# Kernel optimization log

Measured on AMD Instinct MI355X. Metric: run time of the kernel, lower is better.

The kernel has to match this reference:

```python
import jax, jax.numpy as jnp
import numpy as np

N, E, D, H, L, G, C = 50000, 800000, 128, 128, 3, 128, 10
BN_EPS = 1e-5


def setup_inputs() -> dict:
    key = jax.random.key(0)
    ks = jax.random.split(key, 16)
    inp = {
        "x": jax.random.normal(ks[0], (N, D), dtype=jnp.float32),
        "node_centrality": jax.random.uniform(ks[1], (N,), dtype=jnp.float32),
        "edge_centrality": jax.random.uniform(ks[2], (E,), dtype=jnp.float32),
        # stacked per-layer MLP params (in == hidden so stackable)
        "W1": jax.random.normal(ks[3], (L, D, H), dtype=jnp.float32) * 0.05,
        "b1": jnp.zeros((L, H), dtype=jnp.float32),
        "g1": jnp.ones((L, H), dtype=jnp.float32),
        "be1": jnp.zeros((L, H), dtype=jnp.float32),
        "W2": jax.random.normal(ks[4], (L, H, H), dtype=jnp.float32) * 0.05,
        "b2": jnp.zeros((L, H), dtype=jnp.float32),
        "Wc": jax.random.normal(ks[5], (H, C), dtype=jnp.float32) * 0.05,
        "bc": jnp.zeros((C,), dtype=jnp.float32),
        "edge_index": jax.random.randint(ks[6], (2, E), 0, N, dtype=jnp.int64),
        "batch": jnp.sort(jax.random.randint(ks[7], (N,), 0, G, dtype=jnp.int64)),
    }
    return inp


def _gin_forward(x, node_centrality, edge_centrality, W1, b1, g1, be1, W2, b2, Wc, bc, edge_index, batch):
    src, dst = edge_index[0], edge_index[1]  # x_j = x[src], aggregate at dst
    ec = edge_centrality[:, None]
    nc = node_centrality[:, None]
    for l in range(L):
        # message: gather + scale by edge centrality; aggr='add': scatter-add
        msg = x[src] * ec                                      # [E, H]
        agg = jax.ops.segment_sum(msg, dst, num_segments=N)    # [N, H]
        h = agg * nc + x                                       # (1 + eps) * x_r, eps = 0
        # MLP([in, hidden, hidden]): Linear -> BatchNorm(train) -> ReLU -> Linear
        h = h @ W1[l] + b1[l]
        mu = h.mean(axis=0)
        var = h.var(axis=0)  # biased, matches BN training stats
        h = (h - mu) * jax.lax.rsqrt(var + BN_EPS) * g1[l] + be1[l]
        h = jax.nn.relu(h)
        h = h @ W2[l] + b2[l]
        x = jax.nn.relu(h)  # outer .relu() in GIN.forward
    # global mean pool over graphs
    sums = jax.ops.segment_sum(x, batch, num_segments=G)           # [G, H]
    cnt = jax.ops.segment_sum(jnp.ones((N,), x.dtype), batch, num_segments=G)
    pooled = sums / jnp.maximum(cnt, 1.0)[:, None]
    return pooled @ Wc + bc  # [G, C]


def reference(x, edge_index, batch, node_centrality, edge_centrality, W1, b1, g1, be1, W2, b2, Wc, bc):
    return _gin_forward(x, node_centrality, edge_centrality, W1, b1, g1, be1, W2, b2, Wc, bc, edge_index, batch)
```

## Files before the change

### kernel.cpp

```cpp
#include <hip/hip_runtime.h>
#include <hip/hip_fp16.h>

#define Nn 50000
#define Ee 800000
#define HD 128
#define Ll 3
#define Gg 128
#define Cc 10
#define BN_EPS 1e-5f
#define NBLK1 782
#define NPART 1564
#define PPAD 1600
#define NSCB 49

typedef __attribute__((ext_vector_type(8))) __bf16 bf16x8;
typedef __attribute__((ext_vector_type(4))) __bf16 bf16x4;
typedef __attribute__((ext_vector_type(2))) __bf16 bf16x2;
typedef __attribute__((ext_vector_type(4))) float f32x4;

__global__ void k_deg(const int* __restrict__ dst, int* __restrict__ deg) {
  int i = blockIdx.x * blockDim.x + threadIdx.x;
  int base = i * 4;
  if (base >= Ee) return;
#pragma unroll
  for (int j = 0; j < 4; ++j) {
    int e = base + j;
    if (e < Ee) atomicAdd(&deg[dst[e]], 1);
  }
}

__global__ void k_scan1(const int* __restrict__ deg, int* __restrict__ offs,
                        int* __restrict__ bsum) {
  __shared__ int b0[1024], b1[1024];
  int tid = threadIdx.x;
  int i = blockIdx.x * 1024 + tid;
  int v = (i < Nn) ? deg[i] : 0;
  int* cur = b0; int* nxt = b1;
  cur[tid] = v;
  __syncthreads();
  for (int off = 1; off < 1024; off <<= 1) {
    int s = cur[tid] + ((tid >= off) ? cur[tid - off] : 0);
    nxt[tid] = s;
    __syncthreads();
    int* t = cur; cur = nxt; nxt = t;
  }
  if (i < Nn) offs[i] = cur[tid] - v;
  if (tid == 1023) bsum[blockIdx.x] = cur[1023];
}

__global__ void k_scan2(const int* __restrict__ bsum, int* __restrict__ carry) {
  int lane = threadIdx.x;
  int v = (lane < NSCB) ? bsum[lane] : 0;
  int s = v;
  for (int off = 1; off < 64; off <<= 1) {
    int t = __shfl_up(s, off, 64);
    if (lane >= off) s += t;
  }
  if (lane < NSCB) carry[lane] = s - v;
}

__global__ void k_scan3(const int* __restrict__ carry, int* __restrict__ offs,
                        int* __restrict__ cursor) {
  int i = blockIdx.x * 1024 + threadIdx.x;
  if (i < Nn) {
    int o = offs[i] + carry[blockIdx.x];
    offs[i] = o; cursor[i] = o;
  }
  if (i == 0) offs[Nn] = Ee;
}

__global__ void k_fill(const int* __restrict__ src, const int* __restrict__ dst,
                       const float* __restrict__ ec, int* __restrict__ cursor,
                       unsigned int* __restrict__ epk) {
  int i = blockIdx.x * blockDim.x + threadIdx.x;
  int base = i * 4;
  if (base >= Ee) return;
  int d[4], s[4], p[4]; unsigned short hb[4]; bool ok[4];
#pragma unroll
  for (int j = 0; j < 4; ++j) {
    int e = base + j;
    ok[j] = e < Ee;
    if (ok[j]) {
      d[j] = dst[e]; s[j] = src[e];
      hb[j] = __half_as_ushort(__float2half(ec[e]));
    }
  }
#pragma unroll
  for (int j = 0; j < 4; ++j)
    if (ok[j]) p[j] = atomicAdd(&cursor[d[j]], 1);
#pragma unroll
  for (int j = 0; j < 4; ++j)
    if (ok[j]) __builtin_nontemporal_store(((unsigned int)s[j] << 16) | hb[j],
                                           &epk[p[j]]);
}

__global__ void k_xcast(const float* __restrict__ x, __bf16* __restrict__ xb) {
  int i = blockIdx.x * blockDim.x + threadIdx.x;
  int stride = gridDim.x * blockDim.x;
  const int n4 = Nn * 32;
  for (int t = i; t < n4; t += stride) {
    f32x4 v = ((const f32x4*)x)[t];
    bf16x4 b;
#pragma unroll
    for (int j = 0; j < 4; ++j) b[j] = (__bf16)v[j];
    ((bf16x4*)xb)[t] = b;
  }
}

__global__ void k_wprep(const float* __restrict__ W1, const float* __restrict__ W2,
                        __bf16* __restrict__ wtHi, __bf16* __restrict__ wtLo) {
  int mat = blockIdx.x >> 3;
  int chunk = blockIdx.x & 7;
  const float* W = (mat < 3) ? (W1 + mat * 16384) : (W2 + (mat - 3) * 16384);
  __bf16* hi = wtHi + mat * 16384;
  __bf16* lo = wtLo + mat * 16384;
  for (int t = threadIdx.x; t < 2048; t += blockDim.x) {
    int idx = chunk * 2048 + t;
    int n = idx >> 7, k = idx & 127;
    float v = W[k * 128 + n];
    __bf16 h = (__bf16)v;
    hi[idx] = h;
    lo[idx] = (__bf16)(v - (float)h);
  }
}

__global__ void k_agg(const __bf16* __restrict__ xb, const int* __restrict__ offs,
                      const unsigned int* __restrict__ epk, __bf16* __restrict__ aggb) {
  int wid = threadIdx.x >> 6, lane = threadIdx.x & 63;
  int n = blockIdx.x * 4 + wid;
  if (n >= Nn) return;
  int beg = offs[n], end = offs[n + 1];
  const unsigned int* x2 = (const unsigned int*)xb;
  float ax[8], ay[8];
#pragma unroll
  for (int t = 0; t < 8; ++t) { ax[t] = 0.f; ay[t] = 0.f; }
  int j = beg;
  for (; j + 7 < end; j += 8) {
    unsigned int e[8], v[8];
#pragma unroll
    for (int t = 0; t < 8; ++t) e[t] = epk[j + t];
#pragma unroll
    for (int t = 0; t < 8; ++t) v[t] = x2[(e[t] >> 16) * 64 + lane];
#pragma unroll
    for (int t = 0; t < 8; ++t) {
      __half_raw h; h.x = (unsigned short)(e[t] & 0xffffu);
      float w = __half2float(h);
      ax[t] = fmaf(__uint_as_float(v[t] << 16), w, ax[t]);
      ay[t] = fmaf(__uint_as_float(v[t] & 0xffff0000u), w, ay[t]);
    }
  }
  for (; j < end; ++j) {
    unsigned int e = epk[j];
    unsigned int v = x2[(e >> 16) * 64 + lane];
    __half_raw h; h.x = (unsigned short)(e & 0xffffu);
    float w = __half2float(h);
    ax[0] = fmaf(__uint_as_float(v << 16), w, ax[0]);
    ay[0] = fmaf(__uint_as_float(v & 0xffff0000u), w, ay[0]);
  }
  float sx = (ax[0] + ax[1]) + (ax[2] + ax[3]) + ((ax[4] + ax[5]) + (ax[6] + ax[7]));
  float sy = (ay[0] + ay[1]) + (ay[2] + ay[3]) + ((ay[4] + ay[5]) + (ay[6] + ay[7]));
  bf16x2 o; o[0] = (__bf16)sx; o[1] = (__bf16)sy;
  ((bf16x2*)aggb)[n * 64 + lane] = o;
}

__device__ __forceinline__ void split8(const float* a, bf16x8& hi, bf16x8& lo) {
#pragma unroll
  for (int j = 0; j < 8; ++j) {
    float v = a[j];
    __bf16 h = (__bf16)v;
    hi[j] = h;
    lo[j] = (__bf16)(v - (float)h);
  }
}

__launch_bounds__(256)
__global__ void k_gemm1(const __bf16* __restrict__ aggb, const float* __restrict__ nc,
                        const __bf16* __restrict__ xb,
                        const __bf16* __restrict__ wtHi, const __bf16* __restrict__ wtLo,
                        const float* __restrict__ bias, __bf16* __restrict__ h1b,
                        float* __restrict__ partial) {
  int tid = threadIdx.x;
  int w = tid >> 6, l = tid & 63;
  int wr = w >> 1, wc = w & 1;
  int row0 = blockIdx.x * 64 + wr * 32;
  int l15 = l & 15, lg = l >> 4;
  int colw = wc * 64;
  int krow = lg * 8;

  f32x4 acc[2][4];
#pragma unroll
  for (int m = 0; m < 2; ++m)
#pragma unroll
    for (int n = 0; n < 4; ++n) acc[m][n] = (f32x4){0.f, 0.f, 0.f, 0.f};

  int rowA[2]; bool rv[2]; float ncv[2];
#pragma unroll
  for (int m = 0; m < 2; ++m) {
    rowA[m] = row0 + m * 16 + l15;
    rv[m] = rowA[m] < Nn;
    ncv[m] = rv[m] ? nc[rowA[m]] : 0.f;
  }

#pragma unroll
  for (int ks = 0; ks < 4; ++ks) {
    int k0 = ks * 32 + krow;
    bf16x8 aHi[2], aLo[2];
#pragma unroll
    for (int m = 0; m < 2; ++m) {
      float av[8];
      if (rv[m]) {
        bf16x8 ag = *(const bf16x8*)(aggb + rowA[m] * 128 + k0);
        bf16x8 xv = *(const bf16x8*)(xb + rowA[m] * 128 + k0);
#pragma unroll
        for (int jj = 0; jj < 8; ++jj)
          av[jj] = fmaf((float)ag[jj], ncv[m], (float)xv[jj]);
      } else {
#pragma unroll
        for (int jj = 0; jj < 8; ++jj) av[jj] = 0.f;
      }
      split8(av, aHi[m], aLo[m]);
    }
    bf16x8 bHi[4], bLo[4];
#pragma unroll
    for (int n = 0; n < 4; ++n) {
      int c = colw + n * 16 + l15;
      bHi[n] = *(const bf16x8*)(wtHi + c * 128 + k0);
      bLo[n] = *(const bf16x8*)(wtLo + c * 128 + k0);
    }
#pragma unroll
    for (int m = 0; m < 2; ++m)
#pragma unroll
      for (int n = 0; n < 4; ++n) {
        acc[m][n] = __builtin_amdgcn_mfma_f32_16x16x32_bf16(aHi[m], bHi[n], acc[m][n], 0, 0, 0);
        acc[m][n] = __builtin_amdgcn_mfma_f32_16x16x32_bf16(aLo[m], bHi[n], acc[m][n], 0, 0, 0);
        acc[m][n] = __builtin_amdgcn_mfma_f32_16x16x32_bf16(aHi[m], bLo[n], acc[m][n], 0, 0, 0);
      }
  }

  float s[4] = {0.f, 0.f, 0.f, 0.f}, q[4] = {0.f, 0.f, 0.f, 0.f};
#pragma unroll
  for (int n = 0; n < 4; ++n) {
    int c = colw + n * 16 + l15;
    float bv = bias[c];
#pragma unroll
    for (int m = 0; m < 2; ++m) {
      int rbase = row0 + m * 16 + lg * 4;
#pragma unroll
      for (int r = 0; r < 4; ++r) {
        int rr = rbase + r;
        if (rr < Nn) {
          float o = acc[m][n][r] + bv;
          h1b[rr * 128 + c] = (__bf16)o;
          s[n] += o; q[n] += o * o;
        }
      }
    }
  }
#pragma unroll
  for (int n = 0; n < 4; ++n) {
    s[n] += __shfl_xor(s[n], 16, 64); q[n] += __shfl_xor(q[n], 16, 64);
    s[n] += __shfl_xor(s[n], 32, 64); q[n] += __shfl_xor(q[n], 32, 64);
  }
  if (lg == 0) {
    int slot = blockIdx.x * 2 + wr;
#pragma unroll
    for (int n = 0; n < 4; ++n) {
      int f = colw + n * 16 + l15;
      partial[f * PPAD + slot] = s[n];
      partial[(128 + f) * PPAD + slot] = q[n];
    }
  }
}

__global__ void k_bnfin(const float* __restrict__ partial,
                        const float* __restrict__ g1, const float* __restrict__ be1,
                        float* __restrict__ scaleA, float* __restrict__ shiftA) {
  __shared__ float ss[256], qq[256];
  int f = blockIdx.x, t = threadIdx.x;
  float s = 0.f, q = 0.f;
  for (int b = t; b < NPART; b += 256) {
    s += partial[f * PPAD + b];
    q += partial[(128 + f) * PPAD + b];
  }
  ss[t] = s; qq[t] = q;
  __syncthreads();
  for (int off = 128; off > 0; off >>= 1) {
    if (t < off) { ss[t] += ss[t + off]; qq[t] += qq[t + off]; }
    __syncthreads();
  }
  if (t == 0) {
    const float inv = 1.0f / (float)Nn;
    float mu = ss[0] * inv;
    float var = fmaxf(qq[0] * inv - mu * mu, 0.f);
    float rs = rsqrtf(var + BN_EPS);
    float sc = rs * g1[f];
    scaleA[f] = sc;
    shiftA[f] = be1[f] - mu * sc;
  }
}

__launch_bounds__(256)
__global__ void k_gemm2(const __bf16* __restrict__ h1b, const float* __restrict__ scaleA,
                        const float* __restrict__ shiftA,
                        const __bf16* __restrict__ wtHi, const __bf16* __restrict__ wtLo,
                        const float* __restrict__ bias, __bf16* __restrict__ xbout) {
  int tid = threadIdx.x;
  int w = tid >> 6, l = tid & 63;
  int wr = w >> 1, wc = w & 1;
  int row0 = blockIdx.x * 64 + wr * 32;
  int l15 = l & 15, lg = l >> 4;
  int colw = wc * 64;
  int krow = lg * 8;

  f32x4 acc[2][4];
#pragma unroll
  for (int m = 0; m < 2; ++m)
#pragma unroll
    for (int n = 0; n < 4; ++n) acc[m][n] = (f32x4){0.f, 0.f, 0.f, 0.f};

  int rowA[2]; bool rv[2];
#pragma unroll
  for (int m = 0; m < 2; ++m) {
    rowA[m] = row0 + m * 16 + l15;
    rv[m] = rowA[m] < Nn;
  }

#pragma unroll
  for (int ks = 0; ks < 4; ++ks) {
    int k0 = ks * 32 + krow;
    f32x4 sc0 = *(const f32x4*)(scaleA + k0), sc1 = *(const f32x4*)(scaleA + k0 + 4);
    f32x4 sh0 = *(const f32x4*)(shiftA + k0), sh1 = *(const f32x4*)(shiftA + k0 + 4);
    bf16x8 aHi[2], aLo[2];
#pragma unroll
    for (int m = 0; m < 2; ++m) {
      float av[8];
      if (rv[m]) {
        bf16x8 hv = *(const bf16x8*)(h1b + rowA[m] * 128 + k0);
#pragma unroll
        for (int jj = 0; jj < 4; ++jj) {
          av[jj]     = fmaxf(fmaf((float)hv[jj],     sc0[jj], sh0[jj]), 0.f);
          av[4 + jj] = fmaxf(fmaf((float)hv[4 + jj], sc1[jj], sh1[jj]), 0.f);
        }
      } else {
#pragma unroll
        for (int jj = 0; jj < 8; ++jj) av[jj] = 0.f;
      }
      split8(av, aHi[m], aLo[m]);
    }
    bf16x8 bHi[4], bLo[4];
#pragma unroll
    for (int n = 0; n < 4; ++n) {
      int c = colw + n * 16 + l15;
      bHi[n] = *(const bf16x8*)(wtHi + c * 128 + k0);
      bLo[n] = *(const bf16x8*)(wtLo + c * 128 + k0);
    }
#pragma unroll
    for (int m = 0; m < 2; ++m)
#pragma unroll
      for (int n = 0; n < 4; ++n) {
        acc[m][n] = __builtin_amdgcn_mfma_f32_16x16x32_bf16(aHi[m], bHi[n], acc[m][n], 0, 0, 0);
        acc[m][n] = __builtin_amdgcn_mfma_f32_16x16x32_bf16(aLo[m], bHi[n], acc[m][n], 0, 0, 0);
        acc[m][n] = __builtin_amdgcn_mfma_f32_16x16x32_bf16(aHi[m], bLo[n], acc[m][n], 0, 0, 0);
      }
  }

#pragma unroll
  for (int n = 0; n < 4; ++n) {
    int c = colw + n * 16 + l15;
    float bv = bias[c];
#pragma unroll
    for (int m = 0; m < 2; ++m) {
      int rbase = row0 + m * 16 + lg * 4;
#pragma unroll
      for (int r = 0; r < 4; ++r) {
        int rr = rbase + r;
        if (rr < Nn) xbout[rr * 128 + c] = (__bf16)fmaxf(acc[m][n][r] + bv, 0.f);
      }
    }
  }
}

#define PCH 64
__global__ void k_pool(const __bf16* __restrict__ xb, const int* __restrict__ batch,
                       float* __restrict__ pooled, float* __restrict__ gcnt) {
  int wid = threadIdx.x >> 6, lane = threadIdx.x & 63;
  int w = blockIdx.x * 4 + wid;
  int n0 = w * PCH;
  if (n0 >= Nn) return;
  int n1 = (n0 + PCH < Nn) ? n0 + PCH : Nn;
  const unsigned int* x2 = (const unsigned int*)xb;
  float2 acc = make_float2(0.f, 0.f);
  int cur = batch[n0];
  int cnt = 0;
  for (int n = n0; n < n1; ++n) {
    int g = batch[n];
    if (g != cur) {
      atomicAdd(&pooled[cur * 128 + lane * 2 + 0], acc.x);
      atomicAdd(&pooled[cur * 128 + lane * 2 + 1], acc.y);
      if (lane == 0) atomicAdd(&gcnt[cur], (float)cnt);
      acc = make_float2(0.f, 0.f); cnt = 0; cur = g;
    }
    unsigned int v = x2[n * 64 + lane];
    acc.x += __uint_as_float(v << 16);
    acc.y += __uint_as_float(v & 0xffff0000u);
    ++cnt;
  }
  atomicAdd(&pooled[cur * 128 + lane * 2 + 0], acc.x);
  atomicAdd(&pooled[cur * 128 + lane * 2 + 1], acc.y);
  if (lane == 0) atomicAdd(&gcnt[cur], (float)cnt);
}

__global__ void k_head(const float* __restrict__ pooled, const float* __restrict__ gcnt,
                       const float* __restrict__ Wc, const float* __restrict__ bc,
                       float* __restrict__ out) {
  __shared__ float p[128];
  int g = blockIdx.x, tid = threadIdx.x;
  p[tid] = pooled[g * 128 + tid] / fmaxf(gcnt[g], 1.0f);
  __syncthreads();
  if (tid < Cc) {
    float acc = bc[tid];
    for (int k = 0; k < 128; ++k) acc = fmaf(p[k], Wc[k * Cc + tid], acc);
    out[g * Cc + tid] = acc;
  }
}

extern "C" void kernel_launch(void* const* d_in, const int* in_sizes, int n_in,
                              void* d_out, int out_size, void* d_ws, size_t ws_size,
                              hipStream_t stream) {
  const float* x    = (const float*)d_in[0];
  const float* ncn  = (const float*)d_in[1];
  const float* ecn  = (const float*)d_in[2];
  const float* W1   = (const float*)d_in[3];
  const float* b1   = (const float*)d_in[4];
  const float* g1   = (const float*)d_in[5];
  const float* be1  = (const float*)d_in[6];
  const float* W2   = (const float*)d_in[7];
  const float* b2   = (const float*)d_in[8];
  const float* Wc   = (const float*)d_in[9];
  const float* bc   = (const float*)d_in[10];
  const int*   ei   = (const int*)d_in[11];
  const int*   batch= (const int*)d_in[12];
  const int* src  = ei;
  const int* dstp = ei + Ee;

  float* fws = (float*)d_ws;
  float* partial  = fws;
  float* scaleA   = partial + 256 * PPAD;
  float* shiftA   = scaleA + 128;
  float* pooled   = shiftA + 128;
  float* gcnt     = pooled + Gg * 128;
  int*   deg      = (int*)(gcnt + 128);
  int*   offs     = deg + Nn;
  int*   cursor   = offs + Nn + 64;
  int*   bsum     = cursor + Nn;
  int*   carry    = bsum + 64;
  unsigned int* epk = (unsigned int*)(carry + 64);
  __bf16* wtHi    = (__bf16*)(epk + Ee);
  __bf16* wtLo    = wtHi + 6 * 16384;
  __bf16* xb      = wtLo + 6 * 16384;
  __bf16* aggb    = xb + Nn * 128;
  __bf16* h1b     = aggb + Nn * 128;

  k_wprep<<<48, 256, 0, stream>>>(W1, W2, wtHi, wtLo);
  k_xcast<<<2048, 256, 0, stream>>>(x, xb);
  hipMemsetAsync(deg, 0, Nn * sizeof(int), stream);
  k_deg<<<(Ee / 4 + 255) / 256, 256, 0, stream>>>(dstp, deg);
  k_scan1<<<NSCB, 1024, 0, stream>>>(deg, offs, bsum);
  k_scan2<<<1, 64, 0, stream>>>(bsum, carry);
  k_scan3<<<NSCB, 1024, 0, stream>>>(carry, offs, cursor);
  k_fill<<<(Ee / 4 + 255) / 256, 256, 0, stream>>>(src, dstp, ecn, cursor, epk);

  for (int l = 0; l < Ll; ++l) {
    k_agg<<<(Nn + 3) / 4, 256, 0, stream>>>(xb, offs, epk, aggb);
    k_gemm1<<<NBLK1, 256, 0, stream>>>(aggb, ncn, xb,
                                       wtHi + l * 16384, wtLo + l * 16384,
                                       b1 + l * 128, h1b, partial);
    k_bnfin<<<128, 256, 0, stream>>>(partial, g1 + l * 128, be1 + l * 128,
                                     scaleA, shiftA);
    k_gemm2<<<NBLK1, 256, 0, stream>>>(h1b, scaleA, shiftA,
                                       wtHi + (3 + l) * 16384, wtLo + (3 + l) * 16384,
                                       b2 + l * 128, xb);
  }

  hipMemsetAsync(pooled, 0, (Gg * 128 + 128) * sizeof(float), stream);
  k_pool<<<(Nn + PCH * 4 - 1) / (PCH * 4), 256, 0, stream>>>(xb, batch, pooled, gcnt);
  k_head<<<Gg, 128, 0, stream>>>(pooled, gcnt, Wc, bc, (float*)d_out);
}
```

Before: 545.3 us.

## Fuse neighbor aggregation into first GEMM via LDS and drop A-lo MFMA passes

Removes the separate aggregation kernel: each GEMM1 block now gathers and sums neighbor rows for its 64 nodes, combines them with the self term, and stages the bf16 A tile in swizzled shared memory before the MFMA loop. This avoids writing and re-reading the aggregate buffer and saves one launch per layer. Both GEMMs also drop the low-part A split, using a bf16 A operand with hi/lo weights (2 MFMAs instead of 3), which lowers precision. The edge-fill store is made a regular store instead of nontemporal. Risk: the gather phase runs with only 782 blocks, so latency hiding may be worse than in the dedicated aggregation kernel.

Result: slower. 592.8 us (+8.7%).

```diff
diff --git a/kernel.cpp b/kernel.cpp
--- a/kernel.cpp
+++ b/kernel.cpp
@@ -90,8 +90,7 @@
     if (ok[j]) p[j] = atomicAdd(&cursor[d[j]], 1);
 #pragma unroll
   for (int j = 0; j < 4; ++j)
-    if (ok[j]) __builtin_nontemporal_store(((unsigned int)s[j] << 16) | hb[j],
-                                           &epk[p[j]]);
+    if (ok[j]) epk[p[j]] = ((unsigned int)s[j] << 16) | hb[j];
 }
 
 __global__ void k_xcast(const float* __restrict__ x, __bf16* __restrict__ xb) {
@@ -124,68 +123,66 @@
   }
 }
 
-__global__ void k_agg(const __bf16* __restrict__ xb, const int* __restrict__ offs,
-                      const unsigned int* __restrict__ epk, __bf16* __restrict__ aggb) {
-  int wid = threadIdx.x >> 6, lane = threadIdx.x & 63;
-  int n = blockIdx.x * 4 + wid;
-  if (n >= Nn) return;
-  int beg = offs[n], end = offs[n + 1];
-  const unsigned int* x2 = (const unsigned int*)xb;
-  float ax[8], ay[8];
-#pragma unroll
-  for (int t = 0; t < 8; ++t) { ax[t] = 0.f; ay[t] = 0.f; }
-  int j = beg;
-  for (; j + 7 < end; j += 8) {
-    unsigned int e[8], v[8];
-#pragma unroll
-    for (int t = 0; t < 8; ++t) e[t] = epk[j + t];
-#pragma unroll
-    for (int t = 0; t < 8; ++t) v[t] = x2[(e[t] >> 16) * 64 + lane];
-#pragma unroll
-    for (int t = 0; t < 8; ++t) {
-      __half_raw h; h.x = (unsigned short)(e[t] & 0xffffu);
-      float w = __half2float(h);
-      ax[t] = fmaf(__uint_as_float(v[t] << 16), w, ax[t]);
-      ay[t] = fmaf(__uint_as_float(v[t] & 0xffff0000u), w, ay[t]);
-    }
-  }
-  for (; j < end; ++j) {
-    unsigned int e = epk[j];
-    unsigned int v = x2[(e >> 16) * 64 + lane];
-    __half_raw h; h.x = (unsigned short)(e & 0xffffu);
-    float w = __half2float(h);
-    ax[0] = fmaf(__uint_as_float(v << 16), w, ax[0]);
-    ay[0] = fmaf(__uint_as_float(v & 0xffff0000u), w, ay[0]);
-  }
-  float sx = (ax[0] + ax[1]) + (ax[2] + ax[3]) + ((ax[4] + ax[5]) + (ax[6] + ax[7]));
-  float sy = (ay[0] + ay[1]) + (ay[2] + ay[3]) + ((ay[4] + ay[5]) + (ay[6] + ay[7]));
-  bf16x2 o; o[0] = (__bf16)sx; o[1] = (__bf16)sy;
-  ((bf16x2*)aggb)[n * 64 + lane] = o;
-}
-
-__device__ __forceinline__ void split8(const float* a, bf16x8& hi, bf16x8& lo) {
-#pragma unroll
-  for (int j = 0; j < 8; ++j) {
-    float v = a[j];
-    __bf16 h = (__bf16)v;
-    hi[j] = h;
-    lo[j] = (__bf16)(v - (float)h);
-  }
-}
-
 __launch_bounds__(256)
-__global__ void k_gemm1(const __bf16* __restrict__ aggb, const float* __restrict__ nc,
-                        const __bf16* __restrict__ xb,
+__global__ void k_gemm1(const __bf16* __restrict__ xb, const float* __restrict__ nc,
+                        const int* __restrict__ offs, const unsigned int* __restrict__ epk,
                         const __bf16* __restrict__ wtHi, const __bf16* __restrict__ wtLo,
                         const float* __restrict__ bias, __bf16* __restrict__ h1b,
                         float* __restrict__ partial) {
+  __shared__ unsigned int Als[64 * 64];
   int tid = threadIdx.x;
   int w = tid >> 6, l = tid & 63;
+  int row0 = blockIdx.x * 64;
+  const unsigned int* x2 = (const unsigned int*)xb;
+
+  for (int it = 0; it < 16; ++it) {
+    int n = row0 + w * 16 + it;
+    float sx = 0.f, sy = 0.f;
+    if (n < Nn) {
+      int beg = offs[n], end = offs[n + 1];
+      float ax[8], ay[8];
+#pragma unroll
+      for (int t = 0; t < 8; ++t) { ax[t] = 0.f; ay[t] = 0.f; }
+      int j = beg;
+      for (; j + 7 < end; j += 8) {
+        unsigned int e[8], v[8];
+#pragma unroll
+        for (int t = 0; t < 8; ++t) e[t] = epk[j + t];
+#pragma unroll
+        for (int t = 0; t < 8; ++t) v[t] = x2[(e[t] >> 16) * 64 + l];
+#pragma unroll
+        for (int t = 0; t < 8; ++t) {
+          __half_raw h; h.x = (unsigned short)(e[t] & 0xffffu);
+          float wv = __half2float(h);
+          ax[t] = fmaf(__uint_as_float(v[t] << 16), wv, ax[t]);
+          ay[t] = fmaf(__uint_as_float(v[t] & 0xffff0000u), wv, ay[t]);
+        }
+      }
+      for (; j < end; ++j) {
+        unsigned int e = epk[j];
+        unsigned int v = x2[(e >> 16) * 64 + l];
+        __half_raw h; h.x = (unsigned short)(e & 0xffffu);
+        float wv = __half2float(h);
+        ax[0] = fmaf(__uint_as_float(v << 16), wv, ax[0]);
+        ay[0] = fmaf(__uint_as_float(v & 0xffff0000u), wv, ay[0]);
+      }
+      float gx = (ax[0] + ax[1]) + (ax[2] + ax[3]) + ((ax[4] + ax[5]) + (ax[6] + ax[7]));
+      float gy = (ay[0] + ay[1]) + (ay[2] + ay[3]) + ((ay[4] + ay[5]) + (ay[6] + ay[7]));
+      float ncv = nc[n];
+      unsigned int xv = x2[n * 64 + l];
+      sx = fmaf(gx, ncv, __uint_as_float(xv << 16));
+      sy = fmaf(gy, ncv, __uint_as_float(xv & 0xffff0000u));
+    }
+    bf16x2 tpk; tpk[0] = (__bf16)sx; tpk[1] = (__bf16)sy;
+    unsigned int o = *(unsigned int*)&tpk;
+    int sw = (((l >> 2) ^ it) << 2) | (l & 3);
+    Als[(w * 16 + it) * 64 + sw] = o;
+  }
+  __syncthreads();
+
   int wr = w >> 1, wc = w & 1;
-  int row0 = blockIdx.x * 64 + wr * 32;
   int l15 = l & 15, lg = l >> 4;
   int colw = wc * 64;
-  int krow = lg * 8;
 
   f32x4 acc[2][4];
 #pragma unroll
@@ -193,32 +190,15 @@
 #pragma unroll
     for (int n = 0; n < 4; ++n) acc[m][n] = (f32x4){0.f, 0.f, 0.f, 0.f};
 
-  int rowA[2]; bool rv[2]; float ncv[2];
-#pragma unroll
-  for (int m = 0; m < 2; ++m) {
-    rowA[m] = row0 + m * 16 + l15;
-    rv[m] = rowA[m] < Nn;
-    ncv[m] = rv[m] ? nc[rowA[m]] : 0.f;
-  }
-
 #pragma unroll
   for (int ks = 0; ks < 4; ++ks) {
-    int k0 = ks * 32 + krow;
-    bf16x8 aHi[2], aLo[2];
+    int k0 = ks * 32 + lg * 8;
+    bf16x8 a[2];
 #pragma unroll
     for (int m = 0; m < 2; ++m) {
-      float av[8];
-      if (rv[m]) {
-        bf16x8 ag = *(const bf16x8*)(aggb + rowA[m] * 128 + k0);
-        bf16x8 xv = *(const bf16x8*)(xb + rowA[m] * 128 + k0);
-#pragma unroll
-        for (int jj = 0; jj < 8; ++jj)
-          av[jj] = fmaf((float)ag[jj], ncv[m], (float)xv[jj]);
-      } else {
-#pragma unroll
-        for (int jj = 0; jj < 8; ++jj) av[jj] = 0.f;
-      }
-      split8(av, aHi[m], aLo[m]);
+      int lr = wr * 32 + m * 16 + l15;
+      int slot = (((ks * 4 + lg) ^ l15) << 2);
+      a[m] = *(const bf16x8*)&Als[lr * 64 + slot];
     }
     bf16x8 bHi[4], bLo[4];
 #pragma unroll
@@ -231,12 +211,12 @@
     for (int m = 0; m < 2; ++m)
 #pragma unroll
       for (int n = 0; n < 4; ++n) {
-        acc[m][n] = __builtin_amdgcn_mfma_f32_16x16x32_bf16(aHi[m], bHi[n], acc[m][n], 0, 0, 0);
-        acc[m][n] = __builtin_amdgcn_mfma_f32_16x16x32_bf16(aLo[m], bHi[n], acc[m][n], 0, 0, 0);
-        acc[m][n] = __builtin_amdgcn_mfma_f32_16x16x32_bf16(aHi[m], bLo[n], acc[m][n], 0, 0, 0);
-      }
-  }
-
+        acc[m][n] = __builtin_amdgcn_mfma_f32_16x16x32_bf16(a[m], bHi[n], acc[m][n], 0, 0, 0);
+        acc[m][n] = __builtin_amdgcn_mfma_f32_16x16x32_bf16(a[m], bLo[n], acc[m][n], 0, 0, 0);
+      }
+  }
+
+  int row0w = row0 + wr * 32;
   float s[4] = {0.f, 0.f, 0.f, 0.f}, q[4] = {0.f, 0.f, 0.f, 0.f};
 #pragma unroll
   for (int n = 0; n < 4; ++n) {
@@ -244,7 +224,7 @@
     float bv = bias[c];
 #pragma unroll
     for (int m = 0; m < 2; ++m) {
-      int rbase = row0 + m * 16 + lg * 4;
+      int rbase = row0w + m * 16 + lg * 4;
 #pragma unroll
       for (int r = 0; r < 4; ++r) {
         int rr = rbase + r;
@@ -330,22 +310,20 @@
     int k0 = ks * 32 + krow;
     f32x4 sc0 = *(const f32x4*)(scaleA + k0), sc1 = *(const f32x4*)(scaleA + k0 + 4);
     f32x4 sh0 = *(const f32x4*)(shiftA + k0), sh1 = *(const f32x4*)(shiftA + k0 + 4);
-    bf16x8 aHi[2], aLo[2];
+    bf16x8 a[2];
 #pragma unroll
     for (int m = 0; m < 2; ++m) {
-      float av[8];
       if (rv[m]) {
         bf16x8 hv = *(const bf16x8*)(h1b + rowA[m] * 128 + k0);
 #pragma unroll
         for (int jj = 0; jj < 4; ++jj) {
-          av[jj]     = fmaxf(fmaf((float)hv[jj],     sc0[jj], sh0[jj]), 0.f);
-          av[4 + jj] = fmaxf(fmaf((float)hv[4 + jj], sc1[jj], sh1[jj]), 0.f);
+          a[m][jj]     = (__bf16)fmaxf(fmaf((float)hv[jj],     sc0[jj], sh0[jj]), 0.f);
+          a[m][4 + jj] = (__bf16)fmaxf(fmaf((float)hv[4 + jj], sc1[jj], sh1[jj]), 0.f);
         }
       } else {
 #pragma unroll
-        for (int jj = 0; jj < 8; ++jj) av[jj] = 0.f;
-      }
-      split8(av, aHi[m], aLo[m]);
+        for (int jj = 0; jj < 8; ++jj) a[m][jj] = (__bf16)0.f;
+      }
     }
     bf16x8 bHi[4], bLo[4];
 #pragma unroll
@@ -358,9 +336,8 @@
     for (int m = 0; m < 2; ++m)
 #pragma unroll
       for (int n = 0; n < 4; ++n) {
-        acc[m][n] = __builtin_amdgcn_mfma_f32_16x16x32_bf16(aHi[m], bHi[n], acc[m][n], 0, 0, 0);
-        acc[m][n] = __builtin_amdgcn_mfma_f32_16x16x32_bf16(aLo[m], bHi[n], acc[m][n], 0, 0, 0);
-        acc[m][n] = __builtin_amdgcn_mfma_f32_16x16x32_bf16(aHi[m], bLo[n], acc[m][n], 0, 0, 0);
+        acc[m][n] = __builtin_amdgcn_mfma_f32_16x16x32_bf16(a[m], bHi[n], acc[m][n], 0, 0, 0);
+        acc[m][n] = __builtin_amdgcn_mfma_f32_16x16x32_bf16(a[m], bLo[n], acc[m][n], 0, 0, 0);
       }
   }
 
@@ -458,8 +435,7 @@
   __bf16* wtHi    = (__bf16*)(epk + Ee);
   __bf16* wtLo    = wtHi + 6 * 16384;
   __bf16* xb      = wtLo + 6 * 16384;
-  __bf16* aggb    = xb + Nn * 128;
-  __bf16* h1b     = aggb + Nn * 128;
+  __bf16* h1b     = xb + Nn * 128;
 
   k_wprep<<<48, 256, 0, stream>>>(W1, W2, wtHi, wtLo);
   k_xcast<<<2048, 256, 0, stream>>>(x, xb);
@@ -471,8 +447,7 @@
   k_fill<<<(Ee / 4 + 255) / 256, 256, 0, stream>>>(src, dstp, ecn, cursor, epk);
 
   for (int l = 0; l < Ll; ++l) {
-    k_agg<<<(Nn + 3) / 4, 256, 0, stream>>>(xb, offs, epk, aggb);
-    k_gemm1<<<NBLK1, 256, 0, stream>>>(aggb, ncn, xb,
+    k_gemm1<<<NBLK1, 256, 0, stream>>>(xb, ncn, offs, epk,
                                        wtHi + l * 16384, wtLo + l * 16384,
                                        b1 + l * 128, h1b, partial);
     k_bnfin<<<128, 256, 0, stream>>>(partial, g1 + l * 128, be1 + l * 128,
```
